# Optimization experiments

Measured on AMD Instinct MI355X. Metric: run time of the kernel, lower is better.

The kernel has to match this reference:

```python
import jax, jax.numpy as jnp
import numpy as np

N_NODE = 100000
HIDDEN = 128
BATCH = 4096
SESS_LEN = 50


def setup_inputs() -> dict:
    key = jax.random.key(0)
    k1, k2, k3, k4, k5 = jax.random.split(key, 5)
    return {
        "item_embedding": jax.random.normal(k1, (N_NODE, HIDDEN), dtype=jnp.float32),
        "items": jax.random.randint(k2, (BATCH, SESS_LEN), 0, N_NODE, dtype=jnp.int64),
        "A": jax.random.uniform(k3, (BATCH, BATCH), dtype=jnp.float32),
        "D": jax.random.uniform(k4, (BATCH, BATCH), dtype=jnp.float32),
        "target_embedding": jax.random.normal(k5, (BATCH, 1, 2 * HIDDEN), dtype=jnp.float32),
    }


def reference(item_embedding, items, A, D, target_embedding):
    # Gather per-session item embeddings: (batch, sess_len, hidden)
    seq_h = item_embedding[items]
    # Sum over session positions -> (batch, hidden)
    relation_emb = jnp.sum(seq_h, axis=1)
    # DA = D @ A, then propagate: (batch, batch) @ (batch, hidden)
    DA = jnp.matmul(D, A)
    relation_emb = jnp.matmul(DA, relation_emb)
    # Row-wise L2 normalization (torch.norm(dim=-1))
    norm = jnp.linalg.norm(relation_emb, axis=-1, keepdims=True)
    return relation_emb / norm
```

## Files before the change

kernel.cpp:

```cpp
#include <hip/hip_runtime.h>
#include <hip/hip_bf16.h>

#define BATCH   4096
#define HIDDEN  128
#define SESS    50
#define KTOT    4096
#define NB      ((size_t)BATCH * HIDDEN)

#define MB      64
#define KQ      1024
#define BK      64
#define NT      (KQ / BK)
#define ABYTES  16384
#define BBYTES  16384
#define BUF     (ABYTES + BBYTES)

typedef __bf16 bf16x8 __attribute__((ext_vector_type(8)));
typedef float  f32x4  __attribute__((ext_vector_type(4)));
typedef float  f32x2  __attribute__((ext_vector_type(2)));

__device__ __forceinline__ f32x4 mfma_bf16(bf16x8 a, bf16x8 b, f32x4 c) {
    return __builtin_amdgcn_mfma_f32_16x16x32_bf16(a, b, c, 0, 0, 0);
}

__device__ __forceinline__ void gload16(const void* g, void* l) {
    __builtin_amdgcn_global_load_lds(
        (const __attribute__((address_space(1))) void*)g,
        (__attribute__((address_space(3))) void*)l, 16, 0, 0);
}


__global__ __launch_bounds__(256)
void gather_sum_kernel(const float* __restrict__ emb,
                       const int* __restrict__ items32,
                       __bf16* __restrict__ ETp) {
    __shared__ int sidx[4][SESS];
    const int t  = threadIdx.x;
    const int b0 = blockIdx.x * 4;
    const bool is64 = (items32[1] | items32[3] | items32[5] | items32[7] |
                       items32[9] | items32[11] | items32[13] | items32[15]) == 0;
    if (t < 4 * SESS) {
        const int w_ = t / SESS, s_ = t % SESS;
        sidx[w_][s_] = is64
            ? (int)((const long long*)items32)[(long)(b0 + w_) * SESS + s_]
            : items32[(b0 + w_) * SESS + s_];
    }
    __syncthreads();
    const int w    = t >> 6;
    const int lane = t & 63;
    const int c    = lane & 31;
    const int h    = lane >> 5;
    f32x4 acc = {0.f, 0.f, 0.f, 0.f};
#pragma unroll
    for (int i = 0; i < 25; ++i) {
        acc += *(const f32x4*)(emb + (long)sidx[w][h + 2 * i] * HIDDEN + c * 4);
    }
#pragma unroll
    for (int j = 0; j < 4; ++j) acc[j] += __shfl_xor(acc[j], 32, 64);
    if (h == 0) {
        const int  b     = b0 + w;
        const long chunk = b >> 3;
        const int  swz   = (int)((chunk & 3) << 4);
        char* basep = (char*)ETp + chunk * 2048 + (b & 7) * 2;
        const int hi4 = (c >> 2) * 256;
#pragma unroll
        for (int j = 0; j < 4; ++j) {
            const int hl = 4 * (c & 3) + j;
            *(__bf16*)(basep + ((hi4 + hl * 16) ^ swz)) = (__bf16)acc[j];
        }
    }
}

__global__ __launch_bounds__(256, 1)
void gemm_mfma_kernel(const float* __restrict__ X,
                      const __bf16* __restrict__ Bpk,
                      float* __restrict__ Tpart) {
    __shared__ __align__(16) char lds[3 * BUF];
    const int tid  = threadIdx.x;
    const int w    = tid >> 6;
    const int lane = tid & 63;
    const int lo   = lane & 15;
    const int quad = lane >> 4;
    const int rowBase = blockIdx.x * MB;
    const int kq      = blockIdx.y;

#define STAGE(t_, dst_) do {                                                 \
    _Pragma("unroll")                                                        \
    for (int ai_ = 0; ai_ < 4; ++ai_) {                                      \
        const int i_  = 4 * w + ai_;                                         \
        const int rl_ = 4 * i_ + (lane >> 4);           \
        gload16((const char*)X +                                             \
                    ((size_t)(rowBase + rl_) * KTOT + kq * KQ +              \
                     (size_t)(t_) * BK) * 4 +                                \
                    (((lane & 15) * 16) ^ ((rl_ & 7) << 4)),                 \
                (dst_) + i_ * 1024);                                         \
    }                                                                        \
    _Pragma("unroll")                                                        \
    for (int bi_ = 0; bi_ < 4; ++bi_) {                                      \
        const int j_ = 4 * w + bi_;                                          \
        gload16((const char*)Bpk + (size_t)kq * (KQ * 256) +                 \
                    (size_t)(t_) * BBYTES + j_ * 1024 + lane * 16,           \
                (dst_) + ABYTES + j_ * 1024);                                \
    }                                                                        \
} while (0)

    f32x4 acc[8];
#pragma unroll
    for (int i = 0; i < 8; ++i) acc[i] = (f32x4){0.f, 0.f, 0.f, 0.f};

    const int akey = (lo & 7) << 4;
    const int bkey = quad << 4;

#define KTILE(cb_) do {                                                      \
    const char* Ar_ = (cb_) + (16 * w + lo) * 256;                           \
    const char* Bb_ = (cb_) + ABYTES + quad * 2048;                          \
    _Pragma("unroll")                                                        \
    for (int ks_ = 0; ks_ < 2; ++ks_) {                                      \
        const f32x4 a0_ =                                                    \
            *(const f32x4*)(Ar_ + ((ks_ * 128 + quad * 32) ^ akey));         \
        const f32x4 a1_ =                                                    \
            *(const f32x4*)(Ar_ + ((ks_ * 128 + quad * 32 + 16) ^ akey));    \
        bf16x8 af_;                                                          \
        af_[0] = (__bf16)a0_[0]; af_[1] = (__bf16)a0_[1];                    \
        af_[2] = (__bf16)a0_[2]; af_[3] = (__bf16)a0_[3];                    \
        af_[4] = (__bf16)a1_[0]; af_[5] = (__bf16)a1_[1];                    \
        af_[6] = (__bf16)a1_[2]; af_[7] = (__bf16)a1_[3];                    \
        _Pragma("unroll")                                                    \
        for (int j_ = 0; j_ < 8; ++j_) {                                     \
            const bf16x8 b_ = *(const bf16x8*)(Bb_ + ks_ * 8192 +            \
                ((j_ * 256 + lo * 16) ^ bkey));                              \
            acc[j_] = mfma_bf16(af_, b_, acc[j_]);                           \
        }                                                                    \
    }                                                                        \
} while (0)

    STAGE(0, lds);
    STAGE(1, lds + BUF);

    char* cb = lds;
    char* sb = lds + 2 * BUF;
    for (int t = 0; t < NT; ++t) {
        if (t + 2 < NT) STAGE(t + 2, sb);
        if (t < NT - 2)
            asm volatile("s_waitcnt vmcnt(16)" ::: "memory");
        else if (t == NT - 2)
            asm volatile("s_waitcnt vmcnt(8)" ::: "memory");
        else
            asm volatile("s_waitcnt vmcnt(0)" ::: "memory");
        __builtin_amdgcn_s_barrier();
        __builtin_amdgcn_sched_barrier(0);
        KTILE(cb);
        __builtin_amdgcn_s_barrier();
        __builtin_amdgcn_sched_barrier(0);
        cb += BUF; if (cb == lds + 3 * BUF) cb = lds;
        sb += BUF; if (sb == lds + 3 * BUF) sb = lds;
    }
#undef KTILE
#undef STAGE

    float* op = Tpart + (size_t)kq * NB +
                (size_t)(rowBase + 16 * w) * HIDDEN;
#pragma unroll
    for (int r = 0; r < 4; ++r) {
#pragma unroll
        for (int j = 0; j < 8; ++j)
            op[(quad * 4 + r) * HIDDEN + j * 16 + lo] = acc[j][r];
    }
}

__global__ __launch_bounds__(256)
void reduce4_kernel(const float* __restrict__ Tp, __bf16* __restrict__ TTp) {
    const size_t i = ((size_t)blockIdx.x * 256 + threadIdx.x) * 4;
    f32x4 a = *(const f32x4*)(Tp + i);
    a += *(const f32x4*)(Tp + NB + i);
    a += *(const f32x4*)(Tp + 2 * NB + i);
    a += *(const f32x4*)(Tp + 3 * NB + i);
    const int  b     = (int)(i >> 7);
    const int  h0    = (int)(i & 127);
    const long chunk = b >> 3;
    const int  swz   = (int)((chunk & 3) << 4);
    char* basep = (char*)TTp + chunk * 2048 + (b & 7) * 2;
#pragma unroll
    for (int j = 0; j < 4; ++j) {
        const int h = h0 + j;
        *(__bf16*)(basep + (((h >> 4) * 256 + (h & 15) * 16) ^ swz)) =
            (__bf16)a[j];
    }
}

__global__ __launch_bounds__(256)
void reduce_norm_kernel(const float* __restrict__ Tp, float* __restrict__ out) {
    const int t    = threadIdx.x;
    const int w    = t >> 6;
    const int lane = t & 63;
    const int row  = blockIdx.x * 4 + w;
    const size_t base = (size_t)row * HIDDEN + lane * 2;
    f32x2 v = *(const f32x2*)(Tp + base);
    v += *(const f32x2*)(Tp + NB + base);
    v += *(const f32x2*)(Tp + 2 * NB + base);
    v += *(const f32x2*)(Tp + 3 * NB + base);
    float sq = v[0] * v[0] + v[1] * v[1];
#pragma unroll
    for (int m = 1; m < 64; m <<= 1) sq += __shfl_xor(sq, m, 64);
    const float s = rsqrtf(sq);
    f32x2 o = {v[0] * s, v[1] * s};
    *(f32x2*)(out + base) = o;
}

extern "C" void kernel_launch(void* const* d_in, const int* in_sizes, int n_in,
                              void* d_out, int out_size, void* d_ws, size_t ws_size,
                              hipStream_t stream) {
    const float* emb   = (const float*)d_in[0];
    const int*   items = (const int*)d_in[1];
    const float* A     = (const float*)d_in[2];
    const float* D     = (const float*)d_in[3];
    float* out = (float*)d_out;

    __bf16* ETp = (__bf16*)d_ws;
    __bf16* TTp = ETp + NB;
    float*  Tp  = (float*)(TTp + NB);

    gather_sum_kernel<<<BATCH / 4, 256, 0, stream>>>(emb, items, ETp);
    gemm_mfma_kernel<<<dim3(BATCH / MB, 4), 256, 0, stream>>>(A, ETp, Tp);
    reduce4_kernel<<<512, 256, 0, stream>>>(Tp, TTp);
    gemm_mfma_kernel<<<dim3(BATCH / MB, 4), 256, 0, stream>>>(D, TTp, Tp);
    reduce_norm_kernel<<<BATCH / 4, 256, 0, stream>>>(Tp, out);
}
```

Measured before the change: 217.6 us.

## Use 128-row 2x2 warp tiles with 8-way split-K and deeper LDS pipeline

Restructures the GEMM from 64-row tiles with 4-way split-K to 128-row tiles arranged as a 2x2 warp grid (4x4 MFMA fragments per warp), so each loaded A and B fragment is reused more often. The K split goes from 4 to 8 with a smaller K step of 32, and the LDS ring grows to 5 buffers with 4 tiles in flight, dropping the trailing barrier per iteration. The reduce kernels now sum 8 partials, which doubles the partial-sum write and read traffic in exchange for keeping the same 256-block grid with better MFMA density.

```diff
diff --git a/kernel.cpp b/kernel.cpp
--- a/kernel.cpp
+++ b/kernel.cpp
@@ -7,13 +7,15 @@
 #define KTOT    4096
 #define NB      ((size_t)BATCH * HIDDEN)
 
-#define MB      64
-#define KQ      1024
-#define BK      64
-#define NT      (KQ / BK)
-#define ABYTES  16384
-#define BBYTES  16384
-#define BUF     (ABYTES + BBYTES)
+#define MROWS   128
+#define KSP     8
+#define KQL     512
+#define BK      32
+#define NTL     (KQL / BK)
+#define ABY     16384
+#define BBY     8192
+#define BUF     (ABY + BBY)
+#define NBUF    5
 
 typedef __bf16 bf16x8 __attribute__((ext_vector_type(8)));
 typedef float  f32x4  __attribute__((ext_vector_type(4)));
@@ -73,108 +75,118 @@
 
 __global__ __launch_bounds__(256, 1)
 void gemm_mfma_kernel(const float* __restrict__ X,
-                      const __bf16* __restrict__ Bpk,
-                      float* __restrict__ Tpart) {
-    __shared__ __align__(16) char lds[3 * BUF];
+                      const char* __restrict__ Bpk,
+                      float* __restrict__ Tp) {
+    __shared__ __align__(16) char lds[NBUF * BUF];
     const int tid  = threadIdx.x;
     const int w    = tid >> 6;
     const int lane = tid & 63;
     const int lo   = lane & 15;
     const int quad = lane >> 4;
-    const int rowBase = blockIdx.x * MB;
+    const int rowBase = blockIdx.x * MROWS;
     const int kq      = blockIdx.y;
 
-#define STAGE(t_, dst_) do {                                                 \
+    const int mh = w & 1;
+    const int nh = w >> 1;
+    const int akey = (lo & 7) << 4;
+    const int bkey = quad << 4;
+
+#define STG(t_, dst_) do {                                                   \
     _Pragma("unroll")                                                        \
     for (int ai_ = 0; ai_ < 4; ++ai_) {                                      \
         const int i_  = 4 * w + ai_;                                         \
-        const int rl_ = 4 * i_ + (lane >> 4);           \
+        const int rl_ = 8 * i_ + (lane >> 3);          \
         gload16((const char*)X +                                             \
-                    ((size_t)(rowBase + rl_) * KTOT + kq * KQ +              \
+                    ((size_t)(rowBase + rl_) * KTOT + kq * KQL +             \
                      (size_t)(t_) * BK) * 4 +                                \
-                    (((lane & 15) * 16) ^ ((rl_ & 7) << 4)),                 \
+                    ((((lane & 7) * 16)) ^ ((rl_ & 7) << 4)),                \
                 (dst_) + i_ * 1024);                                         \
     }                                                                        \
     _Pragma("unroll")                                                        \
-    for (int bi_ = 0; bi_ < 4; ++bi_) {                                      \
-        const int j_ = 4 * w + bi_;                                          \
-        gload16((const char*)Bpk + (size_t)kq * (KQ * 256) +                 \
-                    (size_t)(t_) * BBYTES + j_ * 1024 + lane * 16,           \
-                (dst_) + ABYTES + j_ * 1024);                                \
+    for (int bi_ = 0; bi_ < 2; ++bi_) {                                      \
+        const int j_ = 2 * w + bi_;                                          \
+        gload16(Bpk + ((size_t)(kq * 64 + (t_) * 4 + (j_ >> 1))) * 2048 +    \
+                    (j_ & 1) * 1024 + lane * 16,                             \
+                (dst_) + ABY + j_ * 1024);                                   \
     }                                                                        \
 } while (0)
 
-    f32x4 acc[8];
-#pragma unroll
-    for (int i = 0; i < 8; ++i) acc[i] = (f32x4){0.f, 0.f, 0.f, 0.f};
-
-    const int akey = (lo & 7) << 4;
-    const int bkey = quad << 4;
-
-#define KTILE(cb_) do {                                                      \
-    const char* Ar_ = (cb_) + (16 * w + lo) * 256;                           \
-    const char* Bb_ = (cb_) + ABYTES + quad * 2048;                          \
-    _Pragma("unroll")                                                        \
-    for (int ks_ = 0; ks_ < 2; ++ks_) {                                      \
-        const f32x4 a0_ =                                                    \
-            *(const f32x4*)(Ar_ + ((ks_ * 128 + quad * 32) ^ akey));         \
+    f32x4 acc[4][4];
+#pragma unroll
+    for (int i = 0; i < 4; ++i)
+#pragma unroll
+        for (int j = 0; j < 4; ++j) acc[i][j] = (f32x4){0.f, 0.f, 0.f, 0.f};
+
+#define KTL(cb_) do {                                                        \
+    const char* Ab_ = (cb_);                                                 \
+    const char* Bb_ = (cb_) + ABY + quad * 2048;                             \
+    bf16x8 af_[4];                                                           \
+    _Pragma("unroll")                                                        \
+    for (int fm_ = 0; fm_ < 4; ++fm_) {                                      \
+        const int rr_ = (mh * 64 + fm_ * 16 + lo) * 128;                     \
+        const f32x4 a0_ = *(const f32x4*)(Ab_ + rr_ + ((quad * 32) ^ akey)); \
         const f32x4 a1_ =                                                    \
-            *(const f32x4*)(Ar_ + ((ks_ * 128 + quad * 32 + 16) ^ akey));    \
-        bf16x8 af_;                                                          \
-        af_[0] = (__bf16)a0_[0]; af_[1] = (__bf16)a0_[1];                    \
-        af_[2] = (__bf16)a0_[2]; af_[3] = (__bf16)a0_[3];                    \
-        af_[4] = (__bf16)a1_[0]; af_[5] = (__bf16)a1_[1];                    \
-        af_[6] = (__bf16)a1_[2]; af_[7] = (__bf16)a1_[3];                    \
+            *(const f32x4*)(Ab_ + rr_ + ((quad * 32 + 16) ^ akey));          \
+        af_[fm_][0] = (__bf16)a0_[0]; af_[fm_][1] = (__bf16)a0_[1];          \
+        af_[fm_][2] = (__bf16)a0_[2]; af_[fm_][3] = (__bf16)a0_[3];          \
+        af_[fm_][4] = (__bf16)a1_[0]; af_[fm_][5] = (__bf16)a1_[1];          \
+        af_[fm_][6] = (__bf16)a1_[2]; af_[fm_][7] = (__bf16)a1_[3];          \
+    }                                                                        \
+    bf16x8 bf_[4];                                                           \
+    _Pragma("unroll")                                                        \
+    for (int fn_ = 0; fn_ < 4; ++fn_)                                        \
+        bf_[fn_] = *(const bf16x8*)(Bb_ +                                    \
+            ((((nh * 4 + fn_) * 256) + lo * 16) ^ bkey));                    \
+    _Pragma("unroll")                                                        \
+    for (int fm_ = 0; fm_ < 4; ++fm_)                                        \
         _Pragma("unroll")                                                    \
-        for (int j_ = 0; j_ < 8; ++j_) {                                     \
-            const bf16x8 b_ = *(const bf16x8*)(Bb_ + ks_ * 8192 +            \
-                ((j_ * 256 + lo * 16) ^ bkey));                              \
-            acc[j_] = mfma_bf16(af_, b_, acc[j_]);                           \
-        }                                                                    \
-    }                                                                        \
+        for (int fn_ = 0; fn_ < 4; ++fn_)                                    \
+            acc[fm_][fn_] = mfma_bf16(af_[fm_], bf_[fn_], acc[fm_][fn_]);    \
 } while (0)
 
-    STAGE(0, lds);
-    STAGE(1, lds + BUF);
-
-    char* cb = lds;
-    char* sb = lds + 2 * BUF;
-    for (int t = 0; t < NT; ++t) {
-        if (t + 2 < NT) STAGE(t + 2, sb);
-        if (t < NT - 2)
-            asm volatile("s_waitcnt vmcnt(16)" ::: "memory");
-        else if (t == NT - 2)
-            asm volatile("s_waitcnt vmcnt(8)" ::: "memory");
+    STG(0, lds + 0 * BUF);
+    STG(1, lds + 1 * BUF);
+    STG(2, lds + 2 * BUF);
+    STG(3, lds + 3 * BUF);
+
+#pragma unroll
+    for (int t = 0; t < NTL; ++t) {
+        if (t <= NTL - 4)
+            asm volatile("s_waitcnt vmcnt(18)" ::: "memory");
+        else if (t == NTL - 3)
+            asm volatile("s_waitcnt vmcnt(12)" ::: "memory");
+        else if (t == NTL - 2)
+            asm volatile("s_waitcnt vmcnt(6)" ::: "memory");
         else
             asm volatile("s_waitcnt vmcnt(0)" ::: "memory");
         __builtin_amdgcn_s_barrier();
         __builtin_amdgcn_sched_barrier(0);
-        KTILE(cb);
-        __builtin_amdgcn_s_barrier();
+        if (t + 4 < NTL) STG(t + 4, lds + ((t + 4) % NBUF) * BUF);
+        KTL(lds + (t % NBUF) * BUF);
         __builtin_amdgcn_sched_barrier(0);
-        cb += BUF; if (cb == lds + 3 * BUF) cb = lds;
-        sb += BUF; if (sb == lds + 3 * BUF) sb = lds;
-    }
-#undef KTILE
-#undef STAGE
-
-    float* op = Tpart + (size_t)kq * NB +
-                (size_t)(rowBase + 16 * w) * HIDDEN;
-#pragma unroll
-    for (int r = 0; r < 4; ++r) {
-#pragma unroll
-        for (int j = 0; j < 8; ++j)
-            op[(quad * 4 + r) * HIDDEN + j * 16 + lo] = acc[j][r];
-    }
+    }
+#undef STG
+#undef KTL
+
+    float* op = Tp + (size_t)kq * NB +
+                (size_t)(rowBase + mh * 64) * HIDDEN + nh * 64;
+#pragma unroll
+    for (int fm = 0; fm < 4; ++fm)
+#pragma unroll
+        for (int r = 0; r < 4; ++r) {
+            const int ro = (fm * 16 + quad * 4 + r) * HIDDEN;
+#pragma unroll
+            for (int fn = 0; fn < 4; ++fn)
+                op[ro + fn * 16 + lo] = acc[fm][fn][r];
+        }
 }
 
 __global__ __launch_bounds__(256)
-void reduce4_kernel(const float* __restrict__ Tp, __bf16* __restrict__ TTp) {
+void reduce8_kernel(const float* __restrict__ Tp, __bf16* __restrict__ TTp) {
     const size_t i = ((size_t)blockIdx.x * 256 + threadIdx.x) * 4;
     f32x4 a = *(const f32x4*)(Tp + i);
-    a += *(const f32x4*)(Tp + NB + i);
-    a += *(const f32x4*)(Tp + 2 * NB + i);
-    a += *(const f32x4*)(Tp + 3 * NB + i);
+#pragma unroll
+    for (int p = 1; p < KSP; ++p) a += *(const f32x4*)(Tp + p * NB + i);
     const int  b     = (int)(i >> 7);
     const int  h0    = (int)(i & 127);
     const long chunk = b >> 3;
@@ -189,16 +201,15 @@
 }
 
 __global__ __launch_bounds__(256)
-void reduce_norm_kernel(const float* __restrict__ Tp, float* __restrict__ out) {
+void rednorm8_kernel(const float* __restrict__ Tp, float* __restrict__ out) {
     const int t    = threadIdx.x;
     const int w    = t >> 6;
     const int lane = t & 63;
     const int row  = blockIdx.x * 4 + w;
     const size_t base = (size_t)row * HIDDEN + lane * 2;
     f32x2 v = *(const f32x2*)(Tp + base);
-    v += *(const f32x2*)(Tp + NB + base);
-    v += *(const f32x2*)(Tp + 2 * NB + base);
-    v += *(const f32x2*)(Tp + 3 * NB + base);
+#pragma unroll
+    for (int p = 1; p < KSP; ++p) v += *(const f32x2*)(Tp + p * NB + base);
     float sq = v[0] * v[0] + v[1] * v[1];
 #pragma unroll
     for (int m = 1; m < 64; m <<= 1) sq += __shfl_xor(sq, m, 64);
@@ -221,8 +232,10 @@
     float*  Tp  = (float*)(TTp + NB);
 
     gather_sum_kernel<<<BATCH / 4, 256, 0, stream>>>(emb, items, ETp);
-    gemm_mfma_kernel<<<dim3(BATCH / MB, 4), 256, 0, stream>>>(A, ETp, Tp);
-    reduce4_kernel<<<512, 256, 0, stream>>>(Tp, TTp);
-    gemm_mfma_kernel<<<dim3(BATCH / MB, 4), 256, 0, stream>>>(D, TTp, Tp);
-    reduce_norm_kernel<<<BATCH / 4, 256, 0, stream>>>(Tp, out);
-}
+    gemm_mfma_kernel<<<dim3(BATCH / MROWS, KSP), 256, 0, stream>>>(
+        A, (const char*)ETp, Tp);
+    reduce8_kernel<<<512, 256, 0, stream>>>(Tp, TTp);
+    gemm_mfma_kernel<<<dim3(BATCH / MROWS, KSP), 256, 0, stream>>>(
+        D, (const char*)TTp, Tp);
+    rednorm8_kernel<<<BATCH / 4, 256, 0, stream>>>(Tp, out);
+}
```

Result: no change. 215.0 us (-1.2%).
